# Performance work log

Measured on AMD Instinct MI355X. Metric: run time of the kernel, lower is better.

## Reference

```python
import jax, jax.numpy as jnp
import numpy as np

D_MODEL = 1024
N_HEAD = 16
B, S = 4, 1024


def _linear(x, W, b):
    # torch nn.Linear: y = x @ W.T + b, W: [out, in]
    return jnp.einsum('bsd,ed->bse', x, W) + b


def _split(x):
    b, s, d = x.shape
    return x.reshape(b, s, N_HEAD, d // N_HEAD).transpose(0, 2, 1, 3)  # [b,h,s,dh]


def _concat(x):
    b, h, s, dh = x.shape
    return x.transpose(0, 2, 1, 3).reshape(b, s, h * dh)


def _attention(q, k, v):
    dh = q.shape[-1]
    scale = 1.0 / np.float32(np.sqrt(dh))
    scores = jnp.einsum('bhqd,bhkd->bhqk', q, k) * scale
    probs = jax.nn.softmax(scores, axis=-1)
    return jnp.einsum('bhqk,bhkd->bhqd', probs, v)


def setup_inputs() -> dict:
    key = jax.random.key(0)
    ks = jax.random.split(key, 20)
    sc = 1.0 / np.float32(np.sqrt(D_MODEL))
    inp = {
        'q': jax.random.normal(ks[0], (B, S, D_MODEL), jnp.float32),
        'k': jax.random.normal(ks[1], (B, S, D_MODEL), jnp.float32),
        'v': jax.random.normal(ks[2], (B, S, D_MODEL), jnp.float32),
    }
    names = ['Wq', 'Wk', 'Wv', 'Wq2', 'Wk2', 'Wv2', 'Wc', 'Wc2']
    for i, n in enumerate(names):
        inp[n] = jax.random.normal(ks[3 + i], (D_MODEL, D_MODEL), jnp.float32) * sc
        inp['b' + n[1:]] = jnp.zeros((D_MODEL,), jnp.float32)
    return inp


def reference(q, k, v, Wq, bq, Wk, bk, Wv, bv, Wq2, bq2, Wk2, bk2, Wv2, bv2, Wc, bc, Wc2, bc2):
    # path 1 projections
    q1 = _linear(q, Wq, bq)
    k1 = _linear(k, Wk, bk)
    v1 = _linear(v, Wv, bv)
    # path 2 projections (note cross-wiring: q2 from k, k2/v2 from q)
    q2 = _linear(k, Wq2, bq2)
    k2 = _linear(q, Wk2, bk2)
    v2 = _linear(q, Wv2, bv2)

    out1 = _attention(_split(q1), _split(k1), _split(v1))
    out2 = _attention(_split(q2), _split(k2), _split(v2))

    out1 = _linear(_concat(out1), Wc, bc)
    out2 = _linear(_concat(out2), Wc2, bc2)
    return out1, out2
```

## Files before the change

### kernel.cpp

```cpp
#include <hip/hip_runtime.h>
#include <hip/hip_bf16.h>

#define B_ 4
#define S_ 1024
#define D_ 1024
#define H_ 16
#define M_ 4096

typedef unsigned short u16;
typedef __attribute__((ext_vector_type(4))) float f32x4;
typedef __attribute__((ext_vector_type(16))) float f32x16;
typedef __attribute__((ext_vector_type(8))) short short8;
typedef __attribute__((ext_vector_type(4))) u16 u16x4;

__device__ inline u16 f2bf(float f) {
  return __builtin_bit_cast(u16, __float2bfloat16(f));
}

__device__ inline short8 ldfrag(const u16* p) {
  return *reinterpret_cast<const short8*>(p);
}

__device__ inline void gload_lds16(const void* g, void* l) {
  __builtin_amdgcn_global_load_lds((const __attribute__((address_space(1))) void*)g,
                                   (__attribute__((address_space(3))) void*)l,
                                   16, 0, 0);
}

__device__ inline int sigma_s(int s) {
  return (s & ~12) | ((s & 4) << 1) | ((s & 8) >> 1);
}

struct GArgs {
  const void* A[6];
  const void* W[6];
  const float* bias[6];
  void* C[6];
  float oscale[6];
  int vtrans[6];
};

struct CvtArgs {
  const float* src[11];
  u16* dst[11];
  int n4[11];
};

__global__ __launch_bounds__(256) void cvt_f32_bf16(CvtArgs a) {
  const int z = blockIdx.y;
  const float4* s = (const float4*)a.src[z];
  u16x4* d = (u16x4*)a.dst[z];
  const int n4 = a.n4[z];
  for (int i = blockIdx.x * blockDim.x + threadIdx.x; i < n4; i += gridDim.x * blockDim.x) {
    float4 v = s[i];
    u16x4 o;
    o[0] = f2bf(v.x); o[1] = f2bf(v.y); o[2] = f2bf(v.z); o[3] = f2bf(v.w);
    d[i] = o;
  }
}

template<typename CT>
__global__ __launch_bounds__(512, 2) void gemm_bt_256(GArgs args) {
  const int z = blockIdx.z;
  const u16* A = (const u16*)args.A[z];
  const u16* W = (const u16*)args.W[z];
  const float* bias = args.bias[z];
  CT* C = (CT*)args.C[z];
  const float oscale = args.oscale[z];
  const int vtrans = args.vtrans[z];

  __shared__ u16 AB[2][2][256 * 64];

  const int tid = threadIdx.x;
  const int lane = tid & 63;
  const int w = tid >> 6;
  const int wm = w >> 2, wn = w & 3;
  const int l15 = lane & 15, lhi = lane >> 4;

  const int lin = blockIdx.x + blockIdx.y * 4;
  const int xcd = lin & 7, idx = lin >> 3;
  const int by = xcd * 2 + (idx >> 2), bx = idx & 3;
  const int m0 = by * 256, n0 = bx * 256;

  const int srow = tid >> 3;
  const int scol = (((tid & 7) ^ ((tid >> 3) & 7)) << 3);

  f32x4 acc[8][4];
#pragma unroll
  for (int m = 0; m < 8; ++m)
#pragma unroll
    for (int n = 0; n < 4; ++n) acc[m][n] = f32x4{0.f, 0.f, 0.f, 0.f};

  {
    const u16* Ag = A + (size_t)m0 * 1024;
    const u16* Wg = W + (size_t)n0 * 1024;
#pragma unroll
    for (int i = 0; i < 4; ++i) {
      gload_lds16(Ag + (size_t)(i * 64 + srow) * 1024 + scol, &AB[0][0][i * 4096 + w * 512]);
      gload_lds16(Wg + (size_t)(i * 64 + srow) * 1024 + scol, &AB[0][1][i * 4096 + w * 512]);
    }
  }

  for (int t = 0; t < 16; ++t) {
    const int db = t & 1;

    asm volatile("s_waitcnt vmcnt(0)" ::: "memory");
    __builtin_amdgcn_s_barrier();
    __builtin_amdgcn_sched_barrier(0);

    if (t < 15) {
      const u16* Ag = A + (size_t)m0 * 1024 + (t + 1) * 64;
      const u16* Wg = W + (size_t)n0 * 1024 + (t + 1) * 64;
#pragma unroll
      for (int i = 0; i < 4; ++i) {
        gload_lds16(Ag + (size_t)(i * 64 + srow) * 1024 + scol, &AB[db ^ 1][0][i * 4096 + w * 512]);
        gload_lds16(Wg + (size_t)(i * 64 + srow) * 1024 + scol, &AB[db ^ 1][1][i * 4096 + w * 512]);
      }
    }

#pragma unroll
    for (int kk = 0; kk < 2; ++kk) {
      short8 af[8], bf4[4];
#pragma unroll
      for (int m = 0; m < 8; ++m) {
        int row = wm * 128 + m * 16 + l15;
        af[m] = ldfrag(&AB[db][0][row * 64 + ((kk * 32 + lhi * 8) ^ ((l15 & 7) << 3))]);
      }
#pragma unroll
      for (int n = 0; n < 4; ++n) {
        int row = wn * 64 + n * 16 + l15;
        bf4[n] = ldfrag(&AB[db][1][row * 64 + ((kk * 32 + lhi * 8) ^ ((l15 & 7) << 3))]);
      }
      __builtin_amdgcn_s_setprio(1);
#pragma unroll
      for (int m = 0; m < 8; ++m)
#pragma unroll
        for (int n = 0; n < 4; ++n)
          acc[m][n] = __builtin_amdgcn_mfma_f32_16x16x32_bf16(af[m], bf4[n], acc[m][n], 0, 0, 0);
      __builtin_amdgcn_s_setprio(0);
    }
  }

#pragma unroll
  for (int m = 0; m < 8; ++m) {
#pragma unroll
    for (int n = 0; n < 4; ++n) {
      int ncol = n0 + wn * 64 + n * 16 + l15;
      float bsv = bias[ncol];
      int mb = m0 + wm * 128 + m * 16 + lhi * 4;
      if (vtrans) {
        int h = ncol >> 6, d = ncol & 63;
        int b = mb >> 10, s0 = sigma_s(mb & 1023);
        u16x4 ov;
#pragma unroll
        for (int r = 0; r < 4; ++r) ov[r] = f2bf((acc[m][n][r] + bsv) * oscale);
        *reinterpret_cast<u16x4*>((u16*)C + ((size_t)((b * 16 + h) * 64 + d)) * 1024 + s0) = ov;
      } else {
#pragma unroll
        for (int r = 0; r < 4; ++r) {
          float val = (acc[m][n][r] + bsv) * oscale;
          if constexpr (sizeof(CT) == 2) ((u16*)C)[(size_t)(mb + r) * 1024 + ncol] = f2bf(val);
          else ((float*)C)[(size_t)(mb + r) * 1024 + ncol] = val;
        }
      }
    }
  }
}

template<typename CT>
__global__ __launch_bounds__(256) void gemm_bt_lds(GArgs args) {
  const int z = blockIdx.z;
  const u16* A = (const u16*)args.A[z];
  const u16* W = (const u16*)args.W[z];
  const float* bias = args.bias[z];
  CT* C = (CT*)args.C[z];
  const float oscale = args.oscale[z];
  const int vtrans = args.vtrans[z];

  __shared__ u16 Al[128 * 64];
  __shared__ u16 Bl[128 * 64];

  const int tid = threadIdx.x;
  const int lane = tid & 63;
  const int w = tid >> 6;
  const int wr = w >> 1, wc = w & 1;
  const int l15 = lane & 15, lhi = lane >> 4;

  const int lin = blockIdx.x + blockIdx.y * 8;
  const int xcd = lin & 7, idx = lin >> 3;
  const int bx = (xcd & 1) * 4 + (idx >> 3);
  const int by = (xcd >> 1) * 8 + (idx & 7);
  const int m0 = by * 128, n0 = bx * 128;

  const int srow = lane >> 3;
  const int scol = (lane & 7) * 8;

  const f32x4 vzero = {0.f, 0.f, 0.f, 0.f};
  f32x4 acc[4][4];
#pragma unroll
  for (int i = 0; i < 4; ++i)
#pragma unroll
    for (int j = 0; j < 4; ++j) acc[i][j] = vzero;

  for (int kt = 0; kt < 1024; kt += 64) {
    __syncthreads();
    const u16* Ag = A + (size_t)m0 * 1024 + kt;
    const u16* Wg = W + (size_t)n0 * 1024 + kt;
#pragma unroll
    for (int j = 0; j < 4; ++j) {
      int rb = w * 32 + j * 8;
      gload_lds16(Ag + (size_t)(rb + srow) * 1024 + scol, &Al[rb * 64]);
      gload_lds16(Wg + (size_t)(rb + srow) * 1024 + scol, &Bl[rb * 64]);
    }
    __syncthreads();

#pragma unroll
    for (int c = 0; c < 2; ++c) {
      short8 af[4], bfr[4];
#pragma unroll
      for (int i = 0; i < 4; ++i) af[i] = ldfrag(&Al[(wr * 64 + i * 16 + l15) * 64 + c * 32 + lhi * 8]);
#pragma unroll
      for (int j = 0; j < 4; ++j) bfr[j] = ldfrag(&Bl[(wc * 64 + j * 16 + l15) * 64 + c * 32 + lhi * 8]);
#pragma unroll
      for (int i = 0; i < 4; ++i)
#pragma unroll
        for (int j = 0; j < 4; ++j)
          acc[i][j] = __builtin_amdgcn_mfma_f32_16x16x32_bf16(af[i], bfr[j], acc[i][j], 0, 0, 0);
    }
  }

#pragma unroll
  for (int i = 0; i < 4; ++i) {
#pragma unroll
    for (int j = 0; j < 4; ++j) {
      int n = n0 + wc * 64 + j * 16 + l15;
      float bsv = bias[n];
      int mb = m0 + wr * 64 + i * 16 + lhi * 4;
      if (vtrans) {
        int h = n >> 6, d = n & 63;
        int b = mb >> 10, s0 = sigma_s(mb & 1023);
        u16x4 ov;
#pragma unroll
        for (int r = 0; r < 4; ++r) ov[r] = f2bf((acc[i][j][r] + bsv) * oscale);
        *reinterpret_cast<u16x4*>((u16*)C + ((size_t)((b * 16 + h) * 64 + d)) * 1024 + s0) = ov;
      } else {
#pragma unroll
        for (int r = 0; r < 4; ++r) {
          float val = (acc[i][j][r] + bsv) * oscale;
          if constexpr (sizeof(CT) == 2) ((u16*)C)[(size_t)(mb + r) * 1024 + n] = f2bf(val);
          else ((float*)C)[(size_t)(mb + r) * 1024 + n] = val;
        }
      }
    }
  }
}

template<typename AT, typename CT>
__global__ __launch_bounds__(256) void gemm_bt_batched(GArgs args) {
  const int z = blockIdx.z;
  const AT* A = (const AT*)args.A[z];
  const float* W = (const float*)args.W[z];
  const float* bias = args.bias[z];
  CT* C = (CT*)args.C[z];
  const float oscale = args.oscale[z];
  const int vtrans = args.vtrans[z];

  __shared__ u16 Al[128][72];
  __shared__ u16 Bl[128][72];

  const int tid = threadIdx.x;
  const int lane = tid & 63;
  const int wid = tid >> 6;
  const int wr = wid >> 1, wc = wid & 1;
  const int m0 = blockIdx.y * 128, n0 = blockIdx.x * 128;
  const int l15 = lane & 15, lhi = lane >> 4;

  const f32x4 vzero = {0.f, 0.f, 0.f, 0.f};
  f32x4 acc[4][4];
#pragma unroll
  for (int i = 0; i < 4; ++i)
#pragma unroll
    for (int j = 0; j < 4; ++j) acc[i][j] = vzero;

  for (int kt = 0; kt < 1024; kt += 64) {
    __syncthreads();
#pragma unroll
    for (int i = 0; i < 8; ++i) {
      int g = tid + i * 256;
      int row = g >> 4, col = (g & 15) * 4;
      u16x4 bv;
      if constexpr (sizeof(AT) == 4) {
        float4 vv = *reinterpret_cast<const float4*>((const float*)A + (size_t)(m0 + row) * 1024 + kt + col);
        bv[0] = f2bf(vv.x); bv[1] = f2bf(vv.y); bv[2] = f2bf(vv.z); bv[3] = f2bf(vv.w);
      } else {
        bv = *reinterpret_cast<const u16x4*>((const u16*)A + (size_t)(m0 + row) * 1024 + kt + col);
      }
      *reinterpret_cast<u16x4*>(&Al[row][col]) = bv;
    }
#pragma unroll
    for (int i = 0; i < 8; ++i) {
      int g = tid + i * 256;
      int row = g >> 4, col = (g & 15) * 4;
      float4 vv = *reinterpret_cast<const float4*>((const float*)W + (size_t)(n0 + row) * 1024 + kt + col);
      u16x4 bv;
      bv[0] = f2bf(vv.x); bv[1] = f2bf(vv.y); bv[2] = f2bf(vv.z); bv[3] = f2bf(vv.w);
      *reinterpret_cast<u16x4*>(&Bl[row][col]) = bv;
    }
    __syncthreads();

#pragma unroll
    for (int c = 0; c < 2; ++c) {
      short8 af[4], bfr[4];
#pragma unroll
      for (int i = 0; i < 4; ++i) af[i] = ldfrag(&Al[wr * 64 + i * 16 + l15][c * 32 + lhi * 8]);
#pragma unroll
      for (int j = 0; j < 4; ++j) bfr[j] = ldfrag(&Bl[wc * 64 + j * 16 + l15][c * 32 + lhi * 8]);
#pragma unroll
      for (int i = 0; i < 4; ++i)
#pragma unroll
        for (int j = 0; j < 4; ++j)
          acc[i][j] = __builtin_amdgcn_mfma_f32_16x16x32_bf16(af[i], bfr[j], acc[i][j], 0, 0, 0);
    }
  }

#pragma unroll
  for (int i = 0; i < 4; ++i) {
#pragma unroll
    for (int j = 0; j < 4; ++j) {
      int n = n0 + wc * 64 + j * 16 + l15;
      float bsv = bias[n];
      int mb = m0 + wr * 64 + i * 16 + lhi * 4;
      if (vtrans) {
        int h = n >> 6, d = n & 63;
        int b = mb >> 10, s0 = sigma_s(mb & 1023);
        u16x4 ov;
#pragma unroll
        for (int r = 0; r < 4; ++r) ov[r] = f2bf((acc[i][j][r] + bsv) * oscale);
        *reinterpret_cast<u16x4*>((u16*)C + ((size_t)((b * 16 + h) * 64 + d)) * 1024 + s0) = ov;
      } else {
#pragma unroll
        for (int r = 0; r < 4; ++r) {
          float val = (acc[i][j][r] + bsv) * oscale;
          if constexpr (sizeof(CT) == 2) ((u16*)C)[(size_t)(mb + r) * 1024 + n] = f2bf(val);
          else ((float*)C)[(size_t)(mb + r) * 1024 + n] = val;
        }
      }
    }
  }
}

__global__ __launch_bounds__(256, 2) void attn_fused32b(const u16* q1b, const u16* k1b, const u16* vt1,
                                                        const u16* q2b, const u16* k2b, const u16* vt2,
                                                        u16* o1, u16* o2) {
  const int qt = blockIdx.x;
  const int h = blockIdx.y;
  const int zb = blockIdx.z;
  const int path = zb >> 2, b = zb & 3;

  const u16* Q = (path == 0) ? q1b : q2b;
  const u16* K = (path == 0) ? k1b : k2b;
  const u16* V = (path == 0) ? vt1 : vt2;
  u16* O = (path == 0) ? o1 : o2;

  const size_t base_qk = (size_t)b * S_ * D_ + (size_t)h * 64;
  const size_t vbase = (size_t)((b * 16 + h) * 64) * 1024;
  const int tid = threadIdx.x;
  const int lane = tid & 63, w = tid >> 6;
  const int lq = lane & 31, hi = lane >> 5;

  __shared__ u16 Ks[2][64][72];
  __shared__ u16 Vs[2][64][72];

  const int srow = tid >> 3;
  const int scol = (tid & 7) * 8;

  const int qbase_row = qt * 256 + w * 64;
  short8 qf[2][4];
#pragma unroll
  for (int qtile = 0; qtile < 2; ++qtile)
#pragma unroll
    for (int dhg = 0; dhg < 4; ++dhg)
      qf[qtile][dhg] = ldfrag(Q + base_qk + (size_t)(qbase_row + qtile * 32 + lq) * 1024 + dhg * 16 + hi * 8);

  f32x16 o_acc[2][2] = {};
  float m_r[2] = {-1e30f, -1e30f};
  float l_r[2] = {0.f, 0.f};

  {
    short8 r0 = ldfrag(K + base_qk + (size_t)srow * 1024 + scol);
    short8 r1 = ldfrag(K + base_qk + (size_t)(srow + 32) * 1024 + scol);
    short8 r2 = ldfrag(V + vbase + (size_t)srow * 1024 + scol);
    short8 r3 = ldfrag(V + vbase + (size_t)(srow + 32) * 1024 + scol);
    *reinterpret_cast<short8*>(&Ks[0][srow][scol]) = r0;
    *reinterpret_cast<short8*>(&Ks[0][srow + 32][scol]) = r1;
    *reinterpret_cast<short8*>(&Vs[0][srow][scol]) = r2;
    *reinterpret_cast<short8*>(&Vs[0][srow + 32][scol]) = r3;
  }
  __syncthreads();

  for (int kv = 0; kv < 16; ++kv) {
    const int cur = kv & 1;

    short8 n0, n1, n2, n3;
    if (kv < 15) {
      const u16* kg = K + base_qk + (size_t)((kv + 1) * 64) * 1024;
      const u16* vg = V + vbase + (kv + 1) * 64;
      n0 = ldfrag(kg + (size_t)srow * 1024 + scol);
      n1 = ldfrag(kg + (size_t)(srow + 32) * 1024 + scol);
      n2 = ldfrag(vg + (size_t)srow * 1024 + scol);
      n3 = ldfrag(vg + (size_t)(srow + 32) * 1024 + scol);
    }

    f32x16 s[2][2] = {};
    __builtin_amdgcn_s_setprio(1);
#pragma unroll
    for (int dhg = 0; dhg < 4; ++dhg) {
#pragma unroll
      for (int keytile = 0; keytile < 2; ++keytile) {
        short8 ka = ldfrag(&Ks[cur][keytile * 32 + lq][dhg * 16 + hi * 8]);
#pragma unroll
        for (int qtile = 0; qtile < 2; ++qtile)
          s[keytile][qtile] = __builtin_amdgcn_mfma_f32_32x32x16_bf16(ka, qf[qtile][dhg], s[keytile][qtile], 0, 0, 0);
      }
    }
    __builtin_amdgcn_s_setprio(0);

#pragma unroll
    for (int qtile = 0; qtile < 2; ++qtile) {
      float pm = s[0][qtile][0];
#pragma unroll
      for (int r = 1; r < 16; ++r) pm = fmaxf(pm, s[0][qtile][r]);
#pragma unroll
      for (int r = 0; r < 16; ++r) pm = fmaxf(pm, s[1][qtile][r]);
      pm = fmaxf(pm, __shfl_xor(pm, 32));
      float mn = fmaxf(m_r[qtile], pm);
      float sc = __expf(m_r[qtile] - mn);
      m_r[qtile] = mn;
      float sum = 0.f;
#pragma unroll
      for (int kt = 0; kt < 2; ++kt)
#pragma unroll
        for (int r = 0; r < 16; ++r) {
          float e = __expf(s[kt][qtile][r] - mn);
          s[kt][qtile][r] = e;
          sum += e;
        }
      sum += __shfl_xor(sum, 32);
      l_r[qtile] = l_r[qtile] * sc + sum;
      o_acc[0][qtile] *= sc;
      o_acc[1][qtile] *= sc;
    }

    __builtin_amdgcn_s_setprio(1);
#pragma unroll
    for (int g = 0; g < 4; ++g) {
      short8 va0 = ldfrag(&Vs[cur][lq][g * 16 + hi * 8]);
      short8 va1 = ldfrag(&Vs[cur][32 + lq][g * 16 + hi * 8]);
#pragma unroll
      for (int qtile = 0; qtile < 2; ++qtile) {
        short8 pb;
#pragma unroll
        for (int j = 0; j < 8; ++j) {
          float pv = (g < 2) ? s[0][qtile][(g & 1) * 8 + j] : s[1][qtile][(g & 1) * 8 + j];
          pb[j] = (short)f2bf(pv);
        }
        o_acc[0][qtile] = __builtin_amdgcn_mfma_f32_32x32x16_bf16(va0, pb, o_acc[0][qtile], 0, 0, 0);
        o_acc[1][qtile] = __builtin_amdgcn_mfma_f32_32x32x16_bf16(va1, pb, o_acc[1][qtile], 0, 0, 0);
      }
    }
    __builtin_amdgcn_s_setprio(0);

    __syncthreads();
    if (kv < 15) {
      const int nxt = cur ^ 1;
      *reinterpret_cast<short8*>(&Ks[nxt][srow][scol]) = n0;
      *reinterpret_cast<short8*>(&Ks[nxt][srow + 32][scol]) = n1;
      *reinterpret_cast<short8*>(&Vs[nxt][srow][scol]) = n2;
      *reinterpret_cast<short8*>(&Vs[nxt][srow + 32][scol]) = n3;
      __syncthreads();
    }
  }

#pragma unroll
  for (int qtile = 0; qtile < 2; ++qtile) {
    float inv = 1.0f / l_r[qtile];
    u16* Op = O + base_qk + (size_t)(qbase_row + qtile * 32 + lq) * 1024;
#pragma unroll
    for (int dtile = 0; dtile < 2; ++dtile) {
#pragma unroll
      for (int qd = 0; qd < 4; ++qd) {
        u16x4 ov;
#pragma unroll
        for (int r = 0; r < 4; ++r) ov[r] = f2bf(o_acc[dtile][qtile][qd * 4 + r] * inv);
        *reinterpret_cast<u16x4*>(Op + dtile * 32 + 8 * qd + 4 * hi) = ov;
      }
    }
  }
}

extern "C" void kernel_launch(void* const* d_in, const int* in_sizes, int n_in,
                              void* d_out, int out_size, void* d_ws, size_t ws_size,
                              hipStream_t stream) {
  const float* q   = (const float*)d_in[0];
  const float* k   = (const float*)d_in[1];
  const float* v   = (const float*)d_in[2];
  const float* Wq  = (const float*)d_in[3];  const float* bq  = (const float*)d_in[4];
  const float* Wk  = (const float*)d_in[5];  const float* bk  = (const float*)d_in[6];
  const float* Wv  = (const float*)d_in[7];  const float* bv  = (const float*)d_in[8];
  const float* Wq2 = (const float*)d_in[9];  const float* bq2 = (const float*)d_in[10];
  const float* Wk2 = (const float*)d_in[11]; const float* bk2 = (const float*)d_in[12];
  const float* Wv2 = (const float*)d_in[13]; const float* bv2 = (const float*)d_in[14];
  const float* Wc  = (const float*)d_in[15]; const float* bc  = (const float*)d_in[16];
  const float* Wc2 = (const float*)d_in[17]; const float* bc2 = (const float*)d_in[18];

  u16* ws = (u16*)d_ws;
  const size_t SZ = (size_t)M_ * D_;
  const size_t WSZ = (size_t)D_ * D_;
  u16* q1b = ws + 0 * SZ;
  u16* k1b = ws + 1 * SZ;
  u16* vt1 = ws + 2 * SZ;
  u16* q2b = ws + 3 * SZ;
  u16* k2b = ws + 4 * SZ;
  u16* vt2 = ws + 5 * SZ;
  u16* a1  = ws + 6 * SZ;
  u16* a2  = ws + 7 * SZ;

  const size_t need = (11 * SZ + 8 * WSZ) * sizeof(u16);

  if (ws_size >= need) {
    u16* qb = ws + 8 * SZ;
    u16* kb = ws + 9 * SZ;
    u16* vb = ws + 10 * SZ;
    u16* wbase = ws + 11 * SZ;
    u16* WqB  = wbase + 0 * WSZ;
    u16* WkB  = wbase + 1 * WSZ;
    u16* WvB  = wbase + 2 * WSZ;
    u16* Wq2B = wbase + 3 * WSZ;
    u16* Wk2B = wbase + 4 * WSZ;
    u16* Wv2B = wbase + 5 * WSZ;
    u16* WcB  = wbase + 6 * WSZ;
    u16* Wc2B = wbase + 7 * WSZ;

    CvtArgs ca;
    ca.src[0] = q;   ca.dst[0] = qb;   ca.n4[0] = (int)(SZ / 4);
    ca.src[1] = k;   ca.dst[1] = kb;   ca.n4[1] = (int)(SZ / 4);
    ca.src[2] = v;   ca.dst[2] = vb;   ca.n4[2] = (int)(SZ / 4);
    ca.src[3] = Wq;  ca.dst[3] = WqB;  ca.n4[3] = (int)(WSZ / 4);
    ca.src[4] = Wk;  ca.dst[4] = WkB;  ca.n4[4] = (int)(WSZ / 4);
    ca.src[5] = Wv;  ca.dst[5] = WvB;  ca.n4[5] = (int)(WSZ / 4);
    ca.src[6] = Wq2; ca.dst[6] = Wq2B; ca.n4[6] = (int)(WSZ / 4);
    ca.src[7] = Wk2; ca.dst[7] = Wk2B; ca.n4[7] = (int)(WSZ / 4);
    ca.src[8] = Wv2; ca.dst[8] = Wv2B; ca.n4[8] = (int)(WSZ / 4);
    ca.src[9] = Wc;  ca.dst[9] = WcB;  ca.n4[9] = (int)(WSZ / 4);
    ca.src[10] = Wc2; ca.dst[10] = Wc2B; ca.n4[10] = (int)(WSZ / 4);
    cvt_f32_bf16<<<dim3(512, 11), dim3(256), 0, stream>>>(ca);

    GArgs pa;
    pa.A[0] = qb; pa.W[0] = WqB;  pa.bias[0] = bq;  pa.C[0] = q1b; pa.oscale[0] = 0.125f; pa.vtrans[0] = 0;
    pa.A[1] = kb; pa.W[1] = WkB;  pa.bias[1] = bk;  pa.C[1] = k1b; pa.oscale[1] = 1.0f;   pa.vtrans[1] = 0;
    pa.A[2] = vb; pa.W[2] = WvB;  pa.bias[2] = bv;  pa.C[2] = vt1; pa.oscale[2] = 1.0f;   pa.vtrans[2] = 1;
    pa.A[3] = kb; pa.W[3] = Wq2B; pa.bias[3] = bq2; pa.C[3] = q2b; pa.oscale[3] = 0.125f; pa.vtrans[3] = 0;
    pa.A[4] = qb; pa.W[4] = Wk2B; pa.bias[4] = bk2; pa.C[4] = k2b; pa.oscale[4] = 1.0f;   pa.vtrans[4] = 0;
    pa.A[5] = qb; pa.W[5] = Wv2B; pa.bias[5] = bv2; pa.C[5] = vt2; pa.oscale[5] = 1.0f;   pa.vtrans[5] = 1;
    gemm_bt_256<u16><<<dim3(4, 16, 6), dim3(512), 0, stream>>>(pa);

    attn_fused32b<<<dim3(4, 16, 8), dim3(256), 0, stream>>>(q1b, k1b, vt1, q2b, k2b, vt2, a1, a2);

    GArgs fa;
    fa.A[0] = a1; fa.W[0] = WcB;  fa.bias[0] = bc;  fa.C[0] = (float*)d_out;      fa.oscale[0] = 1.0f; fa.vtrans[0] = 0;
    fa.A[1] = a2; fa.W[1] = Wc2B; fa.bias[1] = bc2; fa.C[1] = (float*)d_out + SZ; fa.oscale[1] = 1.0f; fa.vtrans[1] = 0;
    gemm_bt_lds<float><<<dim3(8, 32, 2), dim3(256), 0, stream>>>(fa);
  } else {
    GArgs pa;
    pa.A[0] = q; pa.W[0] = Wq;  pa.bias[0] = bq;  pa.C[0] = q1b; pa.oscale[0] = 0.125f; pa.vtrans[0] = 0;
    pa.A[1] = k; pa.W[1] = Wk;  pa.bias[1] = bk;  pa.C[1] = k1b; pa.oscale[1] = 1.0f;   pa.vtrans[1] = 0;
    pa.A[2] = v; pa.W[2] = Wv;  pa.bias[2] = bv;  pa.C[2] = vt1; pa.oscale[2] = 1.0f;   pa.vtrans[2] = 1;
    pa.A[3] = k; pa.W[3] = Wq2; pa.bias[3] = bq2; pa.C[3] = q2b; pa.oscale[3] = 0.125f; pa.vtrans[3] = 0;
    pa.A[4] = q; pa.W[4] = Wk2; pa.bias[4] = bk2; pa.C[4] = k2b; pa.oscale[4] = 1.0f;   pa.vtrans[4] = 0;
    pa.A[5] = q; pa.W[5] = Wv2; pa.bias[5] = bv2; pa.C[5] = vt2; pa.oscale[5] = 1.0f;   pa.vtrans[5] = 1;
    gemm_bt_batched<float, u16><<<dim3(8, 32, 6), dim3(256), 0, stream>>>(pa);

    attn_fused32b<<<dim3(4, 16, 8), dim3(256), 0, stream>>>(q1b, k1b, vt1, q2b, k2b, vt2, a1, a2);

    GArgs fa;
    fa.A[0] = a1; fa.W[0] = Wc;  fa.bias[0] = bc;  fa.C[0] = (float*)d_out;      fa.oscale[0] = 1.0f; fa.vtrans[0] = 0;
    fa.A[1] = a2; fa.W[1] = Wc2; fa.bias[1] = bc2; fa.C[1] = (float*)d_out + SZ; fa.oscale[1] = 1.0f; fa.vtrans[1] = 0;
    gemm_bt_batched<u16, float><<<dim3(8, 32, 2), dim3(256), 0, stream>>>(fa);
  }
}
```

Baseline: 169.3 us.

## Shrink attention per-wave query tile to 32 rows, add lazy rescale and block swizzle

The flash-attention kernel now gives each wave one 32-row query tile instead of two, so a block covers 128 queries and the grid doubles. Launch bounds rise to four blocks per CU. The online softmax skips the rescale of the accumulators when no row max has grown by more than 8, a lazy-rescale trick that keeps accuracy because l and o share the same stale max. Block indices are swizzled so neighbouring blocks share heads for K/V cache reuse. The cost is that K/V LDS tiles are reused across fewer queries, so LDS and global traffic per FLOP roughly doubles.

```diff
diff --git a/kernel.cpp b/kernel.cpp
--- a/kernel.cpp
+++ b/kernel.cpp
@@ -349,11 +349,13 @@
   }
 }
 
-__global__ __launch_bounds__(256, 2) void attn_fused32b(const u16* q1b, const u16* k1b, const u16* vt1,
+__global__ __launch_bounds__(256, 4) void attn_fused32c(const u16* q1b, const u16* k1b, const u16* vt1,
                                                         const u16* q2b, const u16* k2b, const u16* vt2,
                                                         u16* o1, u16* o2) {
-  const int qt = blockIdx.x;
-  const int h = blockIdx.y;
+  const int lin = blockIdx.x + blockIdx.y * 8;
+  const int swz = (lin & 7) * 16 + (lin >> 3);
+  const int qt = swz & 7;
+  const int h = swz >> 3;
   const int zb = blockIdx.z;
   const int path = zb >> 2, b = zb & 3;
 
@@ -374,17 +376,14 @@
   const int srow = tid >> 3;
   const int scol = (tid & 7) * 8;
 
-  const int qbase_row = qt * 256 + w * 64;
-  short8 qf[2][4];
-#pragma unroll
-  for (int qtile = 0; qtile < 2; ++qtile)
-#pragma unroll
-    for (int dhg = 0; dhg < 4; ++dhg)
-      qf[qtile][dhg] = ldfrag(Q + base_qk + (size_t)(qbase_row + qtile * 32 + lq) * 1024 + dhg * 16 + hi * 8);
-
-  f32x16 o_acc[2][2] = {};
-  float m_r[2] = {-1e30f, -1e30f};
-  float l_r[2] = {0.f, 0.f};
+  const int q_row = qt * 128 + w * 32 + lq;
+  short8 qf[4];
+#pragma unroll
+  for (int dhg = 0; dhg < 4; ++dhg)
+    qf[dhg] = ldfrag(Q + base_qk + (size_t)q_row * 1024 + dhg * 16 + hi * 8);
+
+  f32x16 o_acc[2] = {};
+  float m_r = -1e30f, l_r = 0.f;
 
   {
     short8 r0 = ldfrag(K + base_qk + (size_t)srow * 1024 + scol);
@@ -411,62 +410,61 @@
       n3 = ldfrag(vg + (size_t)(srow + 32) * 1024 + scol);
     }
 
-    f32x16 s[2][2] = {};
+    f32x16 s[2] = {};
     __builtin_amdgcn_s_setprio(1);
 #pragma unroll
     for (int dhg = 0; dhg < 4; ++dhg) {
 #pragma unroll
       for (int keytile = 0; keytile < 2; ++keytile) {
         short8 ka = ldfrag(&Ks[cur][keytile * 32 + lq][dhg * 16 + hi * 8]);
-#pragma unroll
-        for (int qtile = 0; qtile < 2; ++qtile)
-          s[keytile][qtile] = __builtin_amdgcn_mfma_f32_32x32x16_bf16(ka, qf[qtile][dhg], s[keytile][qtile], 0, 0, 0);
+        s[keytile] = __builtin_amdgcn_mfma_f32_32x32x16_bf16(ka, qf[dhg], s[keytile], 0, 0, 0);
       }
     }
     __builtin_amdgcn_s_setprio(0);
 
-#pragma unroll
-    for (int qtile = 0; qtile < 2; ++qtile) {
-      float pm = s[0][qtile][0];
-#pragma unroll
-      for (int r = 1; r < 16; ++r) pm = fmaxf(pm, s[0][qtile][r]);
-#pragma unroll
-      for (int r = 0; r < 16; ++r) pm = fmaxf(pm, s[1][qtile][r]);
+    {
+      float pm = s[0][0];
+#pragma unroll
+      for (int r = 1; r < 16; ++r) pm = fmaxf(pm, s[0][r]);
+#pragma unroll
+      for (int r = 0; r < 16; ++r) pm = fmaxf(pm, s[1][r]);
       pm = fmaxf(pm, __shfl_xor(pm, 32));
-      float mn = fmaxf(m_r[qtile], pm);
-      float sc = __expf(m_r[qtile] - mn);
-      m_r[qtile] = mn;
+
+      if (!__all(pm <= m_r + 8.f)) {
+        float mn = fmaxf(m_r, pm);
+        float sc = __expf(m_r - mn);
+        m_r = mn;
+        l_r *= sc;
+        o_acc[0] *= sc;
+        o_acc[1] *= sc;
+      }
+      const float mn = m_r;
       float sum = 0.f;
 #pragma unroll
       for (int kt = 0; kt < 2; ++kt)
 #pragma unroll
         for (int r = 0; r < 16; ++r) {
-          float e = __expf(s[kt][qtile][r] - mn);
-          s[kt][qtile][r] = e;
+          float e = __expf(s[kt][r] - mn);
+          s[kt][r] = e;
           sum += e;
         }
       sum += __shfl_xor(sum, 32);
-      l_r[qtile] = l_r[qtile] * sc + sum;
-      o_acc[0][qtile] *= sc;
-      o_acc[1][qtile] *= sc;
+      l_r += sum;
     }
 
     __builtin_amdgcn_s_setprio(1);
 #pragma unroll
     for (int g = 0; g < 4; ++g) {
+      short8 pb;
+#pragma unroll
+      for (int j = 0; j < 8; ++j) {
+        float pv = (g < 2) ? s[0][(g & 1) * 8 + j] : s[1][(g & 1) * 8 + j];
+        pb[j] = (short)f2bf(pv);
+      }
       short8 va0 = ldfrag(&Vs[cur][lq][g * 16 + hi * 8]);
+      o_acc[0] = __builtin_amdgcn_mfma_f32_32x32x16_bf16(va0, pb, o_acc[0], 0, 0, 0);
       short8 va1 = ldfrag(&Vs[cur][32 + lq][g * 16 + hi * 8]);
-#pragma unroll
-      for (int qtile = 0; qtile < 2; ++qtile) {
-        short8 pb;
-#pragma unroll
-        for (int j = 0; j < 8; ++j) {
-          float pv = (g < 2) ? s[0][qtile][(g & 1) * 8 + j] : s[1][qtile][(g & 1) * 8 + j];
-          pb[j] = (short)f2bf(pv);
-        }
-        o_acc[0][qtile] = __builtin_amdgcn_mfma_f32_32x32x16_bf16(va0, pb, o_acc[0][qtile], 0, 0, 0);
-        o_acc[1][qtile] = __builtin_amdgcn_mfma_f32_32x32x16_bf16(va1, pb, o_acc[1][qtile], 0, 0, 0);
-      }
+      o_acc[1] = __builtin_amdgcn_mfma_f32_32x32x16_bf16(va1, pb, o_acc[1], 0, 0, 0);
     }
     __builtin_amdgcn_s_setprio(0);
 
@@ -481,19 +479,16 @@
     }
   }
 
-#pragma unroll
-  for (int qtile = 0; qtile < 2; ++qtile) {
-    float inv = 1.0f / l_r[qtile];
-    u16* Op = O + base_qk + (size_t)(qbase_row + qtile * 32 + lq) * 1024;
-#pragma unroll
-    for (int dtile = 0; dtile < 2; ++dtile) {
-#pragma unroll
-      for (int qd = 0; qd < 4; ++qd) {
-        u16x4 ov;
-#pragma unroll
-        for (int r = 0; r < 4; ++r) ov[r] = f2bf(o_acc[dtile][qtile][qd * 4 + r] * inv);
-        *reinterpret_cast<u16x4*>(Op + dtile * 32 + 8 * qd + 4 * hi) = ov;
-      }
+  float inv = 1.0f / l_r;
+  u16* Op = O + base_qk + (size_t)q_row * 1024;
+#pragma unroll
+  for (int dtile = 0; dtile < 2; ++dtile) {
+#pragma unroll
+    for (int qd = 0; qd < 4; ++qd) {
+      u16x4 ov;
+#pragma unroll
+      for (int r = 0; r < 4; ++r) ov[r] = f2bf(o_acc[dtile][qd * 4 + r] * inv);
+      *reinterpret_cast<u16x4*>(Op + dtile * 32 + 8 * qd + 4 * hi) = ov;
     }
   }
 }
@@ -564,7 +559,7 @@
     pa.A[5] = qb; pa.W[5] = Wv2B; pa.bias[5] = bv2; pa.C[5] = vt2; pa.oscale[5] = 1.0f;   pa.vtrans[5] = 1;
     gemm_bt_256<u16><<<dim3(4, 16, 6), dim3(512), 0, stream>>>(pa);
 
-    attn_fused32b<<<dim3(4, 16, 8), dim3(256), 0, stream>>>(q1b, k1b, vt1, q2b, k2b, vt2, a1, a2);
+    attn_fused32c<<<dim3(8, 16, 8), dim3(256), 0, stream>>>(q1b, k1b, vt1, q2b, k2b, vt2, a1, a2);
 
     GArgs fa;
     fa.A[0] = a1; fa.W[0] = WcB;  fa.bias[0] = bc;  fa.C[0] = (float*)d_out;      fa.oscale[0] = 1.0f; fa.vtrans[0] = 0;
@@ -580,7 +575,7 @@
     pa.A[5] = q; pa.W[5] = Wv2; pa.bias[5] = bv2; pa.C[5] = vt2; pa.oscale[5] = 1.0f;   pa.vtrans[5] = 1;
     gemm_bt_batched<float, u16><<<dim3(8, 32, 6), dim3(256), 0, stream>>>(pa);
 
-    attn_fused32b<<<dim3(4, 16, 8), dim3(256), 0, stream>>>(q1b, k1b, vt1, q2b, k2b, vt2, a1, a2);
+    attn_fused32c<<<dim3(8, 16, 8), dim3(256), 0, stream>>>(q1b, k1b, vt1, q2b, k2b, vt2, a1, a2);
 
     GArgs fa;
     fa.A[0] = a1; fa.W[0] = Wc;  fa.bias[0] = bc;  fa.C[0] = (float*)d_out;      fa.oscale[0] = 1.0f; fa.vtrans[0] = 0;
```

Result: no change. 169.0 us (-0.2%).
